# Optimization experiments

Hardware: AMD Instinct MI355X
Metric: run time of the kernel (lower is better)

The kernel has to match this reference:

```python
import jax, jax.numpy as jnp
import numpy as np

B, S, E = 4096, 200, 128
ATT_H, MLP_H = 128, 256


def _glorot(key, shape):
    fan_in, fan_out = shape[0], shape[1]
    lim = np.sqrt(6.0 / (fan_in + fan_out)).astype(np.float32)
    return jax.random.uniform(key, shape, jnp.float32, -lim, lim)


def setup_inputs() -> dict:
    key = jax.random.key(0)
    ks = jax.random.split(key, 10)
    return {
        "behavior_emb": jax.random.normal(ks[0], (B, S, E), jnp.float32),
        "candidate_emb": jax.random.normal(ks[1], (B, E), jnp.float32),
        "fc1_w": _glorot(ks[2], (2 * E, ATT_H)),
        "fc1_b": jnp.zeros((ATT_H,), jnp.float32),
        "fc2_w": _glorot(ks[3], (ATT_H, 1)),
        "fc2_b": jnp.zeros((1,), jnp.float32),
        "mlp1_w": _glorot(ks[4], (2 * E, MLP_H)),
        "mlp1_b": jnp.zeros((MLP_H,), jnp.float32),
        "mlp2_w": _glorot(ks[5], (MLP_H, 1)),
        "mlp2_b": jnp.zeros((1,), jnp.float32),
    }


def reference(behavior_emb, candidate_emb, fc1_w, fc1_b, fc2_w, fc2_b,
              mlp1_w, mlp1_b, mlp2_w, mlp2_b):
    # Attention unit: split fc1 weight so we avoid materializing the concat.
    # concat([beh, cand]) @ fc1_w == beh @ W_b + cand @ W_c
    W_b, W_c = fc1_w[:E], fc1_w[E:]
    h = jax.nn.relu(jnp.einsum('bse,eh->bsh', behavior_emb, W_b)
                    + (candidate_emb @ W_c)[:, None, :] + fc1_b)  # [B,S,H]
    scores = jnp.einsum('bsh,h->bs', h, fc2_w[:, 0]) + fc2_b[0]   # [B,S]
    attn = jax.nn.softmax(scores, axis=-1)                         # [B,S]
    user_interest = jnp.einsum('bse,bs->be', behavior_emb, attn)   # [B,E]
    # MLP head
    x = jnp.concatenate([user_interest, candidate_emb], axis=1)    # [B,2E]
    z = jax.nn.relu(x @ mlp1_w + mlp1_b)
    logit = (z @ mlp2_w + mlp2_b)[:, 0]                            # [B]
    return logit
```

## Files before the change

kernel.cpp:

```cpp
#include <hip/hip_runtime.h>
#include <hip/hip_bf16.h>
#include <stdint.h>

#define BN   4096
#define SN   200
#define EN   128
#define HN   128
#define MHN  256
#define RPB  16
#define NBLK (BN / RPB)

typedef __attribute__((ext_vector_type(8)))  short  short8;
typedef __attribute__((ext_vector_type(16))) float  floatx16;

#define SYNC_LGK() do {                                            \
    asm volatile("s_waitcnt lgkmcnt(0)\n\ts_barrier" ::: "memory");\
    __builtin_amdgcn_sched_barrier(0);                             \
  } while (0)
#define ASM_VMCNT0() do {                                          \
    asm volatile("s_waitcnt vmcnt(0)" ::: "memory");               \
    __builtin_amdgcn_sched_barrier(0);                             \
  } while (0)

__device__ __forceinline__ unsigned short f2bf(float f) {
  union { float f; uint32_t u; } c; c.f = f;
  uint32_t r = c.u + 0x7fffu + ((c.u >> 16) & 1u);
  return (unsigned short)(r >> 16);
}
__device__ __forceinline__ float bf2f(unsigned short h) {
  union { uint32_t u; float f; } c; c.u = ((uint32_t)h) << 16;
  return c.f;
}
__device__ __forceinline__ uint32_t pk2(float x, float y) {
#if defined(__has_builtin) && __has_builtin(__builtin_amdgcn_cvt_pk_bf16_f32)
  typedef __bf16 bf16x2 __attribute__((ext_vector_type(2)));
  return __builtin_bit_cast(uint32_t, __builtin_amdgcn_cvt_pk_bf16_f32(x, y));
#else
  return (uint32_t)f2bf(x) | ((uint32_t)f2bf(y) << 16);
#endif
}

__device__ __forceinline__ int aoff(int s, int g) {
  return s * 256 + (((g ^ (s & 15)) << 4));
}

__device__ __forceinline__ void issue_row(const float* __restrict__ src, int tid,
                                          float4 (&va)[13]) {
  #pragma unroll
  for (int u = 0; u < 12; ++u) {
    int q = u * 512 + tid;
    va[u] = *(const float4*)(src + (q >> 5) * EN + ((q & 31) << 2));
  }
  if (tid < 256) {
    int q = 6144 + tid;
    va[12] = *(const float4*)(src + (q >> 5) * EN + ((q & 31) << 2));
  }
}

__device__ __forceinline__ void convert_row(unsigned short* dst, int tid,
                                            const float4 (&va)[13]) {
  #pragma unroll
  for (int u = 0; u < 12; ++u) {
    int q = u * 512 + tid, s = q >> 5, e4 = (q & 31) << 2;
    uint2 pk = make_uint2(pk2(va[u].x, va[u].y), pk2(va[u].z, va[u].w));
    *(uint2*)((char*)dst + s * 256 + ((((e4 >> 3) ^ (s & 15))) << 4) + ((e4 & 7) << 1)) = pk;
  }
  if (tid < 256) {
    int q = 6144 + tid, s = q >> 5, e4 = (q & 31) << 2;
    uint2 pk = make_uint2(pk2(va[12].x, va[12].y), pk2(va[12].z, va[12].w));
    *(uint2*)((char*)dst + s * 256 + ((((e4 >> 3) ^ (s & 15))) << 4) + ((e4 & 7) << 1)) = pk;
  }
}

__global__ __launch_bounds__(512, 2)
void din_fused(const float* __restrict__ behavior, const float* __restrict__ cand,
               const float* __restrict__ fc1w, const float* __restrict__ fc1b,
               const float* __restrict__ fc2w,
               const float* __restrict__ m1w, const float* __restrict__ m1b,
               const float* __restrict__ m2w, const float* __restrict__ m2b,
               float* __restrict__ out) {
  __shared__ unsigned short Abuf[2][SN * EN];
  __shared__ float scores_s[SN];
  __shared__ float cvec_all[RPB][HN];
  __shared__ float cand_all[RPB][EN];
  __shared__ float ui_all[RPB][EN];
  __shared__ float red8[8][8];

  const int tid  = threadIdx.x;
  const int wv   = tid >> 6;
  const int lane = tid & 63;
  const int half = lane >> 5;
  const int l31  = lane & 31;
  const int ht   = wv & 3;
  const int stb  = (wv >> 2) ? 4 : 0;
  const int ste  = (wv >> 2) ? 7 : 4;

  const int base = blockIdx.x * RPB;

  if (tid < SN) scores_s[tid] = 0.f;
  #pragma unroll
  for (int i = tid; i < RPB * EN; i += 512) ((float*)ui_all)[i] = 0.f;
  ((float4*)cand_all)[tid] = ((const float4*)(cand + (size_t)base * EN))[tid];
  __syncthreads();

  float4 va[13];
  issue_row(behavior + (size_t)base * SN * EN, tid, va);

  short8 afr[8];
  #pragma unroll
  for (int t = 0; t < 8; ++t) {
    #pragma unroll
    for (int j = 0; j < 8; ++j) {
      int e = t * 16 + half * 8 + j;
      afr[t][j] = (short)f2bf(fc1w[e * HN + ht * 32 + l31]);
    }
  }
  float wmul[16];
  #pragma unroll
  for (int i = 0; i < 16; ++i) {
    int hr = ht * 32 + (i & 3) + ((i >> 2) << 3) + (half << 2);
    wmul[i] = fc2w[hr];
  }

  {
    const int h  = tid & 127;
    const int r0 = tid >> 7;
    float a0 = fc1b[h], a1 = a0, a2 = a0, a3 = a0;
    const float* wc = fc1w + (size_t)EN * HN + h;
    #pragma unroll 8
    for (int e = 0; e < EN; ++e) {
      float w = wc[(size_t)e * HN];
      a0 = fmaf(cand_all[r0][e],      w, a0);
      a1 = fmaf(cand_all[r0 + 4][e],  w, a1);
      a2 = fmaf(cand_all[r0 + 8][e],  w, a2);
      a3 = fmaf(cand_all[r0 + 12][e], w, a3);
    }
    cvec_all[r0][h]      = a0;
    cvec_all[r0 + 4][h]  = a1;
    cvec_all[r0 + 8][h]  = a2;
    cvec_all[r0 + 12][h] = a3;
  }

  convert_row(Abuf[0], tid, va);
  __syncthreads();

  for (int it = 0; it < RPB; ++it) {
    const int cur = it & 1;

    if (it + 1 < RPB) {
      issue_row(behavior + (size_t)(base + it + 1) * SN * EN, tid, va);
      __builtin_amdgcn_sched_barrier(0);
    }

    float cadd[16];
    #pragma unroll
    for (int i = 0; i < 16; ++i) {
      int hr = ht * 32 + (i & 3) + ((i >> 2) << 3) + (half << 2);
      cadd[i] = cvec_all[it][hr];
    }
    for (int st = stb; st < ste; ++st) {
      floatx16 acc;
      #pragma unroll
      for (int i = 0; i < 16; ++i) acc[i] = cadd[i];
      const int srow = st * 32 + l31;
      const int sr   = (srow < SN) ? srow : (SN - 1);
      #pragma unroll
      for (int t = 0; t < 8; ++t) {
        const short8 bfr = *(const short8*)((const char*)Abuf[cur] + aoff(sr, 2 * t + half));
        acc = __builtin_amdgcn_mfma_f32_32x32x16_bf16(afr[t], bfr, acc, 0, 0, 0);
      }
      float part = 0.f;
      #pragma unroll
      for (int i = 0; i < 16; ++i)
        part = fmaf(fmaxf(acc[i], 0.f), wmul[i], part);
      part += __shfl_xor(part, 32, 64);
      if (lane < 32 && srow < SN) atomicAdd(&scores_s[srow], part);
    }
    SYNC_LGK();

    if (wv == 0) {
      float v0[4];
      #pragma unroll
      for (int k = 0; k < 4; ++k) {
        int s = k * 64 + lane;
        v0[k] = (s < SN) ? scores_s[s] : -3.0e38f;
      }
      float m = fmaxf(fmaxf(v0[0], v0[1]), fmaxf(v0[2], v0[3]));
      #pragma unroll
      for (int off = 32; off >= 1; off >>= 1) m = fmaxf(m, __shfl_xor(m, off, 64));
      float e0[4], sum = 0.f;
      #pragma unroll
      for (int k = 0; k < 4; ++k) { e0[k] = __expf(v0[k] - m); sum += e0[k]; }
      #pragma unroll
      for (int off = 32; off >= 1; off >>= 1) sum += __shfl_xor(sum, off, 64);
      float inv = 1.0f / sum;
      #pragma unroll
      for (int k = 0; k < 4; ++k) {
        int s = k * 64 + lane;
        if (s < SN) scores_s[s] = e0[k] * inv;
      }
    }
    SYNC_LGK();

    {
      const int g  = tid & 15;
      const int sg = tid >> 4;
      float ua[8] = {0.f,0.f,0.f,0.f,0.f,0.f,0.f,0.f};
      for (int s = sg; s < SN; s += 32) {
        float a = scores_s[s];
        const short8 bv = *(const short8*)((const char*)Abuf[cur] + aoff(s, g));
        #pragma unroll
        for (int j = 0; j < 8; ++j) ua[j] = fmaf(a, bf2f((unsigned short)bv[j]), ua[j]);
      }
      #pragma unroll
      for (int j = 0; j < 8; ++j) {
        ua[j] += __shfl_xor(ua[j], 16, 64);
        ua[j] += __shfl_xor(ua[j], 32, 64);
      }
      if (lane < 16) {
        #pragma unroll
        for (int j = 0; j < 8; ++j) atomicAdd(&ui_all[it][(g << 3) + j], ua[j]);
      }
    }
    SYNC_LGK();

    if (tid < SN) scores_s[tid] = 0.f;

    if (it + 1 < RPB) {
      ASM_VMCNT0();
      convert_row(Abuf[cur ^ 1], tid, va);
    }
    SYNC_LGK();
  }

  {
    const int j  = tid & 255;
    const int rh = tid >> 8;
    const float bj = m1b[j];
    float accm[8];
    #pragma unroll
    for (int r = 0; r < 8; ++r) accm[r] = bj;
    #pragma unroll 4
    for (int i = 0; i < 128; ++i) {
      float w = m1w[i * MHN + j];
      #pragma unroll
      for (int r = 0; r < 8; ++r)
        accm[r] = fmaf(ui_all[rh * 8 + r][i], w, accm[r]);
    }
    #pragma unroll 4
    for (int i = 0; i < 128; ++i) {
      float w = m1w[(128 + i) * MHN + j];
      #pragma unroll
      for (int r = 0; r < 8; ++r)
        accm[r] = fmaf(cand_all[rh * 8 + r][i], w, accm[r]);
    }
    const float w2j = m2w[j];
    float prt[8];
    #pragma unroll
    for (int r = 0; r < 8; ++r) prt[r] = fmaxf(accm[r], 0.f) * w2j;
    #pragma unroll
    for (int off = 32; off >= 1; off >>= 1) {
      #pragma unroll
      for (int r = 0; r < 8; ++r) prt[r] += __shfl_xor(prt[r], off, 64);
    }
    if (lane == 0) {
      #pragma unroll
      for (int r = 0; r < 8; ++r) red8[wv][r] = prt[r];
    }
  }
  __syncthreads();
  if (tid < RPB) {
    const int g = tid >> 3, rr = tid & 7;
    float s = red8[g * 4 + 0][rr] + red8[g * 4 + 1][rr]
            + red8[g * 4 + 2][rr] + red8[g * 4 + 3][rr];
    out[base + tid] = s + m2b[0];
  }
}

extern "C" void kernel_launch(void* const* d_in, const int* in_sizes, int n_in,
                              void* d_out, int out_size, void* d_ws, size_t ws_size,
                              hipStream_t stream) {
  const float* behavior = (const float*)d_in[0];
  const float* cand     = (const float*)d_in[1];
  const float* fc1w     = (const float*)d_in[2];
  const float* fc1b     = (const float*)d_in[3];
  const float* fc2w     = (const float*)d_in[4];
  const float* m1w      = (const float*)d_in[6];
  const float* m1b      = (const float*)d_in[7];
  const float* m2w      = (const float*)d_in[8];
  const float* m2b      = (const float*)d_in[9];
  float* outp    = (float*)d_out;

  din_fused<<<NBLK, 512, 0, stream>>>(behavior, cand, fc1w, fc1b, fc2w,
                                      m1w, m1b, m2w, m2b, outp);
}
```

Before: 616.0 us.

## Deepen global prefetch to two rows ahead and fuse softmax into pooling

Behavior rows are now prefetched two iterations ahead using two register buffers that alternate, with partial vmcnt waits so only the older row's loads must finish before conversion. The softmax is now computed redundantly by every wave: each one takes the max and sum itself, and the pooling loop applies exp and normalization as it goes. This removes one block barrier and the single-wave softmax stage. The cost is more registers (26 float4 of staging), which may lower occupancy, plus extra exp work in the pooling loop. The per-wave vmcnt counts depend on issue_row emitting exactly 13 or 12 loads.

```diff
diff --git a/kernel.cpp b/kernel.cpp
--- a/kernel.cpp
+++ b/kernel.cpp
@@ -19,6 +19,11 @@
   } while (0)
 #define ASM_VMCNT0() do {                                          \
     asm volatile("s_waitcnt vmcnt(0)" ::: "memory");               \
+    __builtin_amdgcn_sched_barrier(0);                             \
+  } while (0)
+#define ASM_VMCNT_PREV(wv_) do {                                   \
+    if ((wv_) < 4) asm volatile("s_waitcnt vmcnt(13)" ::: "memory");\
+    else           asm volatile("s_waitcnt vmcnt(12)" ::: "memory");\
     __builtin_amdgcn_sched_barrier(0);                             \
   } while (0)
 
@@ -103,8 +108,8 @@
   ((float4*)cand_all)[tid] = ((const float4*)(cand + (size_t)base * EN))[tid];
   __syncthreads();
 
-  float4 va[13];
-  issue_row(behavior + (size_t)base * SN * EN, tid, va);
+  float4 vaA[13], vaB[13];
+  issue_row(behavior + (size_t)base * SN * EN, tid, vaA);
 
   short8 afr[8];
   #pragma unroll
@@ -141,14 +146,15 @@
     cvec_all[r0 + 12][h] = a3;
   }
 
-  convert_row(Abuf[0], tid, va);
-  __syncthreads();
-
-  for (int it = 0; it < RPB; ++it) {
+  convert_row(Abuf[0], tid, vaA);
+  issue_row(behavior + (size_t)(base + 1) * SN * EN, tid, vaB);
+  SYNC_LGK();
+
+  auto body = [&](int it, float4 (&vaI)[13], float4 (&vaC)[13]) {
     const int cur = it & 1;
 
-    if (it + 1 < RPB) {
-      issue_row(behavior + (size_t)(base + it + 1) * SN * EN, tid, va);
+    if (it + 2 < RPB) {
+      issue_row(behavior + (size_t)(base + it + 2) * SN * EN, tid, vaI);
       __builtin_amdgcn_sched_barrier(0);
     }
 
@@ -178,36 +184,28 @@
     }
     SYNC_LGK();
 
-    if (wv == 0) {
+    {
       float v0[4];
       #pragma unroll
       for (int k = 0; k < 4; ++k) {
-        int s = k * 64 + lane;
+        int s = (lane << 2) + k;
         v0[k] = (s < SN) ? scores_s[s] : -3.0e38f;
       }
       float m = fmaxf(fmaxf(v0[0], v0[1]), fmaxf(v0[2], v0[3]));
       #pragma unroll
       for (int off = 32; off >= 1; off >>= 1) m = fmaxf(m, __shfl_xor(m, off, 64));
-      float e0[4], sum = 0.f;
-      #pragma unroll
-      for (int k = 0; k < 4; ++k) { e0[k] = __expf(v0[k] - m); sum += e0[k]; }
+      float sum = 0.f;
+      #pragma unroll
+      for (int k = 0; k < 4; ++k) sum += __expf(v0[k] - m);
       #pragma unroll
       for (int off = 32; off >= 1; off >>= 1) sum += __shfl_xor(sum, off, 64);
-      float inv = 1.0f / sum;
-      #pragma unroll
-      for (int k = 0; k < 4; ++k) {
-        int s = k * 64 + lane;
-        if (s < SN) scores_s[s] = e0[k] * inv;
-      }
-    }
-    SYNC_LGK();
-
-    {
+      const float inv = 1.0f / sum;
+
       const int g  = tid & 15;
       const int sg = tid >> 4;
       float ua[8] = {0.f,0.f,0.f,0.f,0.f,0.f,0.f,0.f};
       for (int s = sg; s < SN; s += 32) {
-        float a = scores_s[s];
+        float a = __expf(scores_s[s] - m) * inv;
         const short8 bv = *(const short8*)((const char*)Abuf[cur] + aoff(s, g));
         #pragma unroll
         for (int j = 0; j < 8; ++j) ua[j] = fmaf(a, bf2f((unsigned short)bv[j]), ua[j]);
@@ -227,10 +225,16 @@
     if (tid < SN) scores_s[tid] = 0.f;
 
     if (it + 1 < RPB) {
-      ASM_VMCNT0();
-      convert_row(Abuf[cur ^ 1], tid, va);
+      if (it + 2 < RPB) { ASM_VMCNT_PREV(wv); }
+      else              { ASM_VMCNT0();       }
+      convert_row(Abuf[cur ^ 1], tid, vaC);
     }
     SYNC_LGK();
+  };
+
+  for (int it2 = 0; it2 < RPB; it2 += 2) {
+    body(it2,     vaA, vaB);
+    body(it2 + 1, vaB, vaA);
   }
 
   {
```

Result: slower. 684.7 us (+11.2%).
